# Kernel tuning notes

Measured on AMD Instinct MI355X. Metric: run time of the kernel, lower is better.

## Reference

```python
import jax, jax.numpy as jnp
import numpy as np

N, C, H, W = 16, 256, 48, 96
S = 64   # num_s = 2*num_state_mid; also num_n = mids*mids = 64 (must match)
EPS = 1e-5


def setup_inputs() -> dict:
    key = jax.random.key(0)
    ks = jax.random.split(key, 11)
    sc = 0.05
    return {
        "x": jax.random.normal(ks[0], (N, C, H, W), jnp.float32),
        "edge": jax.random.normal(ks[1], (N, 2, H, W), jnp.float32),
        # conv_state: Conv2d(C, S, 1) with bias
        "Ws": jax.random.normal(ks[2], (S, C), jnp.float32) * sc,
        "bs": jax.random.normal(ks[3], (S,), jnp.float32) * sc,
        # conv_proj: Conv2d(C, S, 1) with bias
        "Wp": jax.random.normal(ks[4], (S, C), jnp.float32) * sc,
        "bp": jax.random.normal(ks[5], (S,), jnp.float32) * sc,
        # GCN conv1: Conv1d(num_n, num_n, 1, bias=False)
        "W1": jax.random.normal(ks[6], (S, S), jnp.float32) * sc,
        # GCN conv2: Conv1d(S, S, 1, bias=False)
        "W2": jax.random.normal(ks[7], (S, S), jnp.float32) * sc,
        # conv_extend: Conv2d(S, C, 1, bias=False)
        "We": jax.random.normal(ks[8], (C, S), jnp.float32) * sc,
        # BatchNorm2d(C) affine params (training-mode batch stats used in forward)
        "gamma": jnp.ones((C,), jnp.float32),
        "beta": jnp.zeros((C,), jnp.float32),
    }


def reference(x, edge, Ws, bs, Wp, bp, W1, W2, We, gamma, beta):
    n, c, h, w = x.shape
    s = Ws.shape[0]
    # edge softmax over channels, take class-1 probability map  -> (n,1,h,w)
    edge_g = jax.nn.softmax(edge, axis=1)[:, 1:2]

    # 1x1 convs as channel matmuls
    xs = jnp.einsum('oc,nchw->nohw', Ws, x) + bs[None, :, None, None]
    xs = xs.reshape(n, s, h * w)                        # (n,S,HW)
    xp = jnp.einsum('oc,nchw->nohw', Wp, x) + bp[None, :, None, None]
    # x_proj_region + x_proj_edge == xp * (1 + edge_gate)
    comb = (xp * (1.0 + edge_g)).reshape(n, s, h * w)
    comb = jax.nn.softmax(comb, axis=-1)                # softmax over spatial

    # project to graph space: (n,S,HW) @ (n,HW,S) -> (n,S,S)
    xn = jnp.einsum('nsk,ntk->nst', xs, comb)

    # GCN: conv1 over node dim (last axis mixes via W1), subtract, conv2 over state dim, relu
    hh = jnp.einsum('ij,nsj->nsi', W1, xn) - xn
    hh = jax.nn.relu(jnp.einsum('ij,njk->nik', W2, hh))

    # back-project: (n,S,S) @ (n,S,HW) -> (n,S,HW) -> (n,S,H,W)
    xr = jnp.einsum('nst,ntk->nsk', hh, comb).reshape(n, s, h, w)

    # conv_extend (no bias) then BatchNorm2d in training mode (biased batch var)
    ext = jnp.einsum('os,nshw->nohw', We, xr)
    mean = ext.mean(axis=(0, 2, 3), keepdims=True)
    var = ext.var(axis=(0, 2, 3), keepdims=True)
    bn = gamma[None, :, None, None] * (ext - mean) * jax.lax.rsqrt(var + EPS) \
         + beta[None, :, None, None]
    return x + bn
```

## Files before the change

kernel.cpp:

```cpp
#include <hip/hip_runtime.h>

#define HW 4608
#define NB 16
#define CC 256
#define SS 64
#define EPS 1e-5f
#define NSPLIT 24

typedef __attribute__((ext_vector_type(8))) short short8;
typedef __attribute__((ext_vector_type(4))) float f32x4;

__device__ __forceinline__ ushort f2bf(float f) {
    uint u = __float_as_uint(f);
    return (ushort)((u + 0x7FFFu + ((u >> 16) & 1u)) >> 16);
}
__device__ __forceinline__ float bf2f(ushort h) {
    return __uint_as_float(((uint)h) << 16);
}

__global__ __launch_bounds__(256) void k_wf(const float* __restrict__ Ws,
                                            const float* __restrict__ Wp,
                                            ushort* __restrict__ Wf) {
    int idx = blockIdx.x * 256 + threadIdx.x;
    int j = idx & 7, r = (idx >> 3) & 127, kq = (idx >> 10) & 3, cs = idx >> 12;
    int c = cs * 32 + kq * 8 + j;
    float v = (r < 64) ? Ws[r * CC + c] : Wp[(r - 64) * CC + c];
    Wf[idx] = f2bf(v);
}

__global__ __launch_bounds__(256) void k_proj(const float* __restrict__ x,
                                              const ushort* __restrict__ Wf,
                                              const float* __restrict__ bs,
                                              const float* __restrict__ bp,
                                              const float* __restrict__ edge,
                                              ushort* __restrict__ xsb,
                                              ushort* __restrict__ Eb,
                                              float* __restrict__ rsum) {
    __shared__ __align__(16) ushort Bl[4 * 64 * 8];
    int n = blockIdx.y, k0 = blockIdx.x * 64;
    int tid = threadIdx.x, lane = tid & 63, w = tid >> 6;
    int q = lane >> 4, li = lane & 15;
    f32x4 acc[2][4] = {};
    const float* xb = x + (size_t)n * CC * HW + k0 + lane;
    float pf[8];
    uint4 afn[2];
#pragma unroll
    for (int j = 0; j < 8; j++) pf[j] = xb[(size_t)(w * 8 + j) * HW];
#pragma unroll
    for (int mt = 0; mt < 2; mt++)
        afn[mt] = *(const uint4*)&Wf[((0 * 4 + q) * 128 + w * 32 + mt * 16 + li) * 8];
#pragma unroll 1
    for (int cs = 0; cs < 8; cs++) {
        union { ushort u[8]; uint4 v; } tmp;
#pragma unroll
        for (int j = 0; j < 8; j++) tmp.u[j] = f2bf(pf[j]);
        short8 af[2];
        af[0] = *(short8*)&afn[0];
        af[1] = *(short8*)&afn[1];
        *(uint4*)&Bl[(w * 64 + lane) * 8] = tmp.v;
        __syncthreads();
        if (cs < 7) {
#pragma unroll
            for (int j = 0; j < 8; j++)
                pf[j] = xb[(size_t)((cs + 1) * 32 + w * 8 + j) * HW];
#pragma unroll
            for (int mt = 0; mt < 2; mt++)
                afn[mt] = *(const uint4*)&Wf[(((cs + 1) * 4 + q) * 128 + w * 32 + mt * 16 + li) * 8];
        }
        short8 bfr[4];
#pragma unroll
        for (int nt = 0; nt < 4; nt++) {
            uint4 t = *(const uint4*)&Bl[(q * 64 + nt * 16 + li) * 8];
            bfr[nt] = *(short8*)&t;
        }
#pragma unroll
        for (int mt = 0; mt < 2; mt++)
#pragma unroll
            for (int nt = 0; nt < 4; nt++)
                acc[mt][nt] = __builtin_amdgcn_mfma_f32_16x16x32_bf16(af[mt], bfr[nt], acc[mt][nt], 0, 0, 0);
        __syncthreads();
    }
    if (w < 2) {
#pragma unroll
        for (int mt = 0; mt < 2; mt++) {
#pragma unroll
            for (int rr = 0; rr < 4; rr++) {
                int s = w * 32 + mt * 16 + q * 4 + rr;
                float bv = bs[s];
#pragma unroll
                for (int nt = 0; nt < 4; nt++) {
                    int col = k0 + nt * 16 + li;
                    xsb[((size_t)n * SS + s) * HW + col] = f2bf(acc[mt][nt][rr] + bv);
                }
            }
        }
    } else {
        float ga[4];
#pragma unroll
        for (int nt = 0; nt < 4; nt++) {
            int col = k0 + nt * 16 + li;
            float e0 = edge[((size_t)n * 2 + 0) * HW + col];
            float e1 = edge[((size_t)n * 2 + 1) * HW + col];
            ga[nt] = 1.f + 1.f / (1.f + __expf(e0 - e1));
        }
        float rp[2][4];
#pragma unroll
        for (int mt = 0; mt < 2; mt++) {
#pragma unroll
            for (int rr = 0; rr < 4; rr++) {
                int s = (w - 2) * 32 + mt * 16 + q * 4 + rr;
                float bv = bp[s];
                float sum = 0.f;
#pragma unroll
                for (int nt = 0; nt < 4; nt++) {
                    int col = k0 + nt * 16 + li;
                    float e = __expf((acc[mt][nt][rr] + bv) * ga[nt]);
                    sum += e;
                    Eb[((size_t)n * SS + s) * HW + col] = f2bf(e);
                }
                rp[mt][rr] = sum;
            }
        }
#pragma unroll
        for (int b = 1; b < 16; b <<= 1)
#pragma unroll
            for (int mt = 0; mt < 2; mt++)
#pragma unroll
                for (int rr = 0; rr < 4; rr++)
                    rp[mt][rr] += __shfl_xor(rp[mt][rr], b, 64);
        if (li == 0) {
#pragma unroll
            for (int mt = 0; mt < 2; mt++)
#pragma unroll
                for (int rr = 0; rr < 4; rr++)
                    atomicAdd(&rsum[n * SS + (w - 2) * 32 + mt * 16 + q * 4 + rr], rp[mt][rr]);
        }
    }
}

__global__ __launch_bounds__(256) void k_graph(const ushort* __restrict__ xsb,
                                               const ushort* __restrict__ Eb,
                                               float* __restrict__ U,
                                               float* __restrict__ P) {
    int n = blockIdx.y, sp = blockIdx.x;
    int kbase = sp * (HW / NSPLIT);
    int tid = threadIdx.x, lane = tid & 63, w = tid >> 6;
    int q = lane >> 4, li = lane & 15;
    bool isP = w >= 2;
    int half = w & 1;
    const ushort* Arow = isP ? Eb : xsb;
    f32x4 acc[2][4] = {};
    for (int ks = 0; ks < (HW / NSPLIT) / 32; ks++) {
        int kb = kbase + ks * 32 + q * 8;
        short8 af[2], bfr[4];
#pragma unroll
        for (int mt = 0; mt < 2; mt++) {
            int s = half * 32 + mt * 16 + li;
            uint4 t = *(const uint4*)&Arow[((size_t)n * SS + s) * HW + kb];
            af[mt] = *(short8*)&t;
        }
#pragma unroll
        for (int nt = 0; nt < 4; nt++) {
            int tt = nt * 16 + li;
            uint4 t = *(const uint4*)&Eb[((size_t)n * SS + tt) * HW + kb];
            bfr[nt] = *(short8*)&t;
        }
#pragma unroll
        for (int mt = 0; mt < 2; mt++)
#pragma unroll
            for (int nt = 0; nt < 4; nt++)
                acc[mt][nt] = __builtin_amdgcn_mfma_f32_16x16x32_bf16(af[mt], bfr[nt], acc[mt][nt], 0, 0, 0);
    }
    float* dst = (isP ? P : U) + (size_t)n * 4096;
#pragma unroll
    for (int mt = 0; mt < 2; mt++)
#pragma unroll
        for (int nt = 0; nt < 4; nt++)
#pragma unroll
            for (int rr = 0; rr < 4; rr++) {
                int row = half * 32 + mt * 16 + q * 4 + rr;
                int col = nt * 16 + li;
                atomicAdd(&dst[row * 64 + col], acc[mt][nt][rr]);
            }
}

__global__ __launch_bounds__(256) void k_gcn(const float* __restrict__ U,
                                             const float* __restrict__ rsum,
                                             const float* __restrict__ W1,
                                             const float* __restrict__ W2,
                                             const float* __restrict__ We,
                                             float* __restrict__ M,
                                             ushort* __restrict__ Mf) {
    __shared__ __align__(16) float A[64 * 68];
    __shared__ __align__(16) float B[64 * 68];
    __shared__ __align__(16) float Cb[64 * 68];
    __shared__ float rs[64];
    int n = blockIdx.x;
    int cc = blockIdx.y;
    int tid = threadIdx.x;
    int t0 = tid >> 4, t1 = tid & 15;
    if (tid < 64) rs[tid] = 1.0f / rsum[n * SS + tid];
    __syncthreads();
#pragma unroll
    for (int i = 0; i < 16; i++) {
        int idx = tid + i * 256;
        int r = idx >> 6, cth = idx & 63;
        A[cth * 68 + r] = U[n * 4096 + idx] * rs[cth];
        B[cth * 68 + r] = W1[idx];
    }
    __syncthreads();
    {
        float acc[4][4] = {};
        for (int j = 0; j < 64; j++) {
            float4 a4 = *(const float4*)&A[j * 68 + t0 * 4];
            float4 b4 = *(const float4*)&B[j * 68 + t1 * 4];
            float a[4] = {a4.x, a4.y, a4.z, a4.w};
            float b[4] = {b4.x, b4.y, b4.z, b4.w};
#pragma unroll
            for (int p = 0; p < 4; p++)
#pragma unroll
                for (int qq = 0; qq < 4; qq++) acc[p][qq] += a[p] * b[qq];
        }
#pragma unroll
        for (int p = 0; p < 4; p++)
#pragma unroll
            for (int qq = 0; qq < 4; qq++) {
                acc[p][qq] -= A[(t1 * 4 + qq) * 68 + (t0 * 4 + p)];
                Cb[(t0 * 4 + p) * 68 + t1 * 4 + qq] = acc[p][qq];
            }
    }
    __syncthreads();
#pragma unroll
    for (int i = 0; i < 16; i++) {
        int idx = tid + i * 256;
        int r = idx >> 6, cth = idx & 63;
        B[cth * 68 + r] = W2[idx];
    }
    __syncthreads();
    {
        float acc[4][4] = {};
        for (int j = 0; j < 64; j++) {
            float4 a4 = *(const float4*)&B[j * 68 + t0 * 4];
            float4 b4 = *(const float4*)&Cb[j * 68 + t1 * 4];
            float a[4] = {a4.x, a4.y, a4.z, a4.w};
            float b[4] = {b4.x, b4.y, b4.z, b4.w};
#pragma unroll
            for (int p = 0; p < 4; p++)
#pragma unroll
                for (int qq = 0; qq < 4; qq++) acc[p][qq] += a[p] * b[qq];
        }
        __syncthreads();
#pragma unroll
        for (int p = 0; p < 4; p++)
#pragma unroll
            for (int qq = 0; qq < 4; qq++)
                A[(t0 * 4 + p) * 68 + t1 * 4 + qq] = fmaxf(acc[p][qq], 0.f);
    }
    __syncthreads();
#pragma unroll
    for (int i = 0; i < 16; i++) {
        int idx = tid + i * 256;
        int c = idx >> 6, j = idx & 63;
        B[j * 68 + c] = We[(cc * 64 + c) * 64 + j];
    }
    __syncthreads();
    {
        float acc[4][4] = {};
        for (int j = 0; j < 64; j++) {
            float4 a4 = *(const float4*)&B[j * 68 + t0 * 4];
            float4 b4 = *(const float4*)&A[j * 68 + t1 * 4];
            float a[4] = {a4.x, a4.y, a4.z, a4.w};
            float b[4] = {b4.x, b4.y, b4.z, b4.w};
#pragma unroll
            for (int p = 0; p < 4; p++)
#pragma unroll
                for (int qq = 0; qq < 4; qq++) acc[p][qq] += a[p] * b[qq];
        }
#pragma unroll
        for (int p = 0; p < 4; p++) {
            int c = cc * 64 + t0 * 4 + p;
            float v[4];
#pragma unroll
            for (int qq = 0; qq < 4; qq++) v[qq] = acc[p][qq] * rs[t1 * 4 + qq];
            float4 st = {v[0], v[1], v[2], v[3]};
            *(float4*)&M[((size_t)n * CC + c) * 64 + t1 * 4] = st;
#pragma unroll
            for (int qq = 0; qq < 4; qq++) {
                int t = t1 * 4 + qq;
                Mf[(size_t)n * 16384 + ((t >> 3) * 256 + c) * 8 + (t & 7)] = f2bf(v[qq]);
            }
        }
    }
}

__global__ __launch_bounds__(256) void k_stats(const float* __restrict__ M,
                                               const float* __restrict__ P,
                                               const float* __restrict__ rsum,
                                               const float* __restrict__ gamma,
                                               const float* __restrict__ beta,
                                               float* __restrict__ sc,
                                               float* __restrict__ bi) {
    __shared__ float ms[NB][64];
    __shared__ float red[256];
    int c = blockIdx.x;
    int tid = threadIdx.x;
    for (int i = tid; i < NB * 64; i += 256) {
        int n = i >> 6, s = i & 63;
        ms[n][s] = M[((size_t)n * CC + c) * 64 + s];
    }
    __syncthreads();
    float qa = 0.f;
    for (int n = 0; n < NB; n++) {
        const float* Pn = P + n * 4096;
#pragma unroll
        for (int p = 0; p < 16; p++) {
            int e = p * 256 + tid;
            qa += ms[n][e >> 6] * ms[n][e & 63] * Pn[e];
        }
    }
    float sa = 0.f;
    for (int i = tid; i < NB * 64; i += 256) {
        int n = i >> 6, s = i & 63;
        sa += ms[n][s] * rsum[n * SS + s];
    }
    red[tid] = qa;
    __syncthreads();
    for (int off = 128; off > 0; off >>= 1) {
        if (tid < off) red[tid] += red[tid + off];
        __syncthreads();
    }
    float qtot = red[0];
    __syncthreads();
    red[tid] = sa;
    __syncthreads();
    for (int off = 128; off > 0; off >>= 1) {
        if (tid < off) red[tid] += red[tid + off];
        __syncthreads();
    }
    if (tid == 0) {
        float stot = red[0];
        const float invM = 1.0f / ((float)NB * (float)HW);
        float mean = stot * invM;
        float var = qtot * invM - mean * mean;
        float s = gamma[c] * rsqrtf(var + EPS);
        sc[c] = s;
        bi[c] = beta[c] - s * mean;
    }
}

__global__ __launch_bounds__(256) void k_out(const float* __restrict__ x,
                                             const ushort* __restrict__ Mf,
                                             const ushort* __restrict__ Eb,
                                             const float* __restrict__ sc,
                                             const float* __restrict__ bi,
                                             float* __restrict__ out) {
    __shared__ __align__(16) ushort Bl[8 * 64 * 8];
    int n = blockIdx.y, k0 = blockIdx.x * 64;
    int tid = threadIdx.x, lane = tid & 63, w = tid >> 6;
    int q = lane >> 4, li = lane & 15;
    {
        int nl = tid & 63, pr = tid >> 6;
#pragma unroll
        for (int kk = 0; kk < 2; kk++) {
            int kq = pr * 2 + kk;
            union { ushort u[8]; uint4 v; } tmp;
#pragma unroll
            for (int j = 0; j < 8; j++)
                tmp.u[j] = Eb[((size_t)n * SS + kq * 8 + j) * HW + k0 + nl];
            *(uint4*)&Bl[(kq * 64 + nl) * 8] = tmp.v;
        }
    }
    __syncthreads();
    f32x4 acc[4][4] = {};
#pragma unroll
    for (int ks = 0; ks < 2; ks++) {
        short8 af[4], bfr[4];
#pragma unroll
        for (int mt = 0; mt < 4; mt++) {
            int c = w * 64 + mt * 16 + li;
            uint4 t = *(const uint4*)&Mf[(size_t)n * 16384 + ((ks * 4 + q) * 256 + c) * 8];
            af[mt] = *(short8*)&t;
        }
#pragma unroll
        for (int nt = 0; nt < 4; nt++) {
            int nl = nt * 16 + li;
            uint4 t = *(const uint4*)&Bl[((ks * 4 + q) * 64 + nl) * 8];
            bfr[nt] = *(short8*)&t;
        }
#pragma unroll
        for (int mt = 0; mt < 4; mt++)
#pragma unroll
            for (int nt = 0; nt < 4; nt++)
                acc[mt][nt] = __builtin_amdgcn_mfma_f32_16x16x32_bf16(af[mt], bfr[nt], acc[mt][nt], 0, 0, 0);
    }
#pragma unroll
    for (int mt = 0; mt < 4; mt++) {
#pragma unroll
        for (int rr = 0; rr < 4; rr++) {
            int c = w * 64 + mt * 16 + q * 4 + rr;
            float s_ = sc[c], bv = bi[c];
            size_t base = ((size_t)n * CC + c) * HW + k0;
#pragma unroll
            for (int nt = 0; nt < 4; nt++) {
                int col = nt * 16 + li;
                out[base + col] = x[base + col] + s_ * acc[mt][nt][rr] + bv;
            }
        }
    }
}

extern "C" void kernel_launch(void* const* d_in, const int* in_sizes, int n_in,
                              void* d_out, int out_size, void* d_ws, size_t ws_size,
                              hipStream_t stream) {
    const float* x = (const float*)d_in[0];
    const float* edge = (const float*)d_in[1];
    const float* Ws = (const float*)d_in[2];
    const float* bs = (const float*)d_in[3];
    const float* Wp = (const float*)d_in[4];
    const float* bp = (const float*)d_in[5];
    const float* W1 = (const float*)d_in[6];
    const float* W2 = (const float*)d_in[7];
    const float* We = (const float*)d_in[8];
    const float* gamma = (const float*)d_in[9];
    const float* beta = (const float*)d_in[10];
    float* out = (float*)d_out;

    char* base = (char*)d_ws;
    ushort* Wf  = (ushort*)base;                    base += 65536;
    ushort* xsb = (ushort*)base;                    base += 9437184;
    ushort* Eb  = (ushort*)base;                    base += 9437184;
    float*  rsum= (float*)base;                     base += 4096;
    float*  U   = (float*)base;                     base += 262144;
    float*  P   = (float*)base;                     base += 262144;
    float*  M   = (float*)base;                     base += 1048576;
    ushort* Mf  = (ushort*)base;                    base += 524288;
    float*  sc  = (float*)base;                     base += 1024;
    float*  bi  = (float*)base;                     base += 1024;

    hipMemsetAsync(rsum, 0, 4096 + 262144 + 262144, stream);
    k_wf<<<128, 256, 0, stream>>>(Ws, Wp, Wf);
    k_proj<<<dim3(72, NB), 256, 0, stream>>>(x, Wf, bs, bp, edge, xsb, Eb, rsum);
    k_graph<<<dim3(NSPLIT, NB), 256, 0, stream>>>(xsb, Eb, U, P);
    k_gcn<<<dim3(NB, 4), 256, 0, stream>>>(U, rsum, W1, W2, We, M, Mf);
    k_stats<<<256, 256, 0, stream>>>(M, P, rsum, gamma, beta, sc, bi);
    k_out<<<dim3(72, NB), 256, 0, stream>>>(x, Mf, Eb, sc, bi, out);
}
```

Measured before the change: 223.4 us.

## Double-buffer projection LDS tile and vectorize output epilogue through shared staging

```diff
diff --git a/kernel.cpp b/kernel.cpp
--- a/kernel.cpp
+++ b/kernel.cpp
@@ -36,7 +36,7 @@
                                               ushort* __restrict__ xsb,
                                               ushort* __restrict__ Eb,
                                               float* __restrict__ rsum) {
-    __shared__ __align__(16) ushort Bl[4 * 64 * 8];
+    __shared__ __align__(16) ushort Bl[2][4 * 64 * 8];
     int n = blockIdx.y, k0 = blockIdx.x * 64;
     int tid = threadIdx.x, lane = tid & 63, w = tid >> 6;
     int q = lane >> 4, li = lane & 15;
@@ -49,16 +49,18 @@
 #pragma unroll
     for (int mt = 0; mt < 2; mt++)
         afn[mt] = *(const uint4*)&Wf[((0 * 4 + q) * 128 + w * 32 + mt * 16 + li) * 8];
-#pragma unroll 1
+#pragma unroll 2
     for (int cs = 0; cs < 8; cs++) {
+        int b = cs & 1;
         union { ushort u[8]; uint4 v; } tmp;
 #pragma unroll
         for (int j = 0; j < 8; j++) tmp.u[j] = f2bf(pf[j]);
         short8 af[2];
         af[0] = *(short8*)&afn[0];
         af[1] = *(short8*)&afn[1];
-        *(uint4*)&Bl[(w * 64 + lane) * 8] = tmp.v;
-        __syncthreads();
+        *(uint4*)&Bl[b][(w * 64 + lane) * 8] = tmp.v;
+        asm volatile("s_waitcnt lgkmcnt(0)" ::: "memory");
+        __builtin_amdgcn_s_barrier();
         if (cs < 7) {
 #pragma unroll
             for (int j = 0; j < 8; j++)
@@ -70,7 +72,7 @@
         short8 bfr[4];
 #pragma unroll
         for (int nt = 0; nt < 4; nt++) {
-            uint4 t = *(const uint4*)&Bl[(q * 64 + nt * 16 + li) * 8];
+            uint4 t = *(const uint4*)&Bl[b][(q * 64 + nt * 16 + li) * 8];
             bfr[nt] = *(short8*)&t;
         }
 #pragma unroll
@@ -78,7 +80,6 @@
 #pragma unroll
             for (int nt = 0; nt < 4; nt++)
                 acc[mt][nt] = __builtin_amdgcn_mfma_f32_16x16x32_bf16(af[mt], bfr[nt], acc[mt][nt], 0, 0, 0);
-        __syncthreads();
     }
     if (w < 2) {
 #pragma unroll
@@ -354,57 +355,73 @@
                                              const float* __restrict__ sc,
                                              const float* __restrict__ bi,
                                              float* __restrict__ out) {
-    __shared__ __align__(16) ushort Bl[8 * 64 * 8];
-    int n = blockIdx.y, k0 = blockIdx.x * 64;
+    __shared__ __align__(16) char shb[64 * 132 * 4];
+    ushort* Bl = (ushort*)shb;
+    float* E2 = (float*)shb;
+    int n = blockIdx.y;
+    int kt = blockIdx.x >> 1, ct = blockIdx.x & 1;
+    int k0 = kt * 128, c0 = ct * 128;
     int tid = threadIdx.x, lane = tid & 63, w = tid >> 6;
     int q = lane >> 4, li = lane & 15;
     {
-        int nl = tid & 63, pr = tid >> 6;
-#pragma unroll
-        for (int kk = 0; kk < 2; kk++) {
-            int kq = pr * 2 + kk;
+        int nl = tid & 127, pr = tid >> 7;
+#pragma unroll
+        for (int kk = 0; kk < 4; kk++) {
+            int kq = pr * 4 + kk;
             union { ushort u[8]; uint4 v; } tmp;
 #pragma unroll
             for (int j = 0; j < 8; j++)
                 tmp.u[j] = Eb[((size_t)n * SS + kq * 8 + j) * HW + k0 + nl];
-            *(uint4*)&Bl[(kq * 64 + nl) * 8] = tmp.v;
-        }
-    }
-    __syncthreads();
-    f32x4 acc[4][4] = {};
+            *(uint4*)&Bl[(kq * 128 + nl) * 8] = tmp.v;
+        }
+    }
+    __syncthreads();
+    f32x4 acc[2][8] = {};
 #pragma unroll
     for (int ks = 0; ks < 2; ks++) {
-        short8 af[4], bfr[4];
-#pragma unroll
-        for (int mt = 0; mt < 4; mt++) {
-            int c = w * 64 + mt * 16 + li;
+        short8 af[2], bfr[8];
+#pragma unroll
+        for (int mt = 0; mt < 2; mt++) {
+            int c = c0 + w * 32 + mt * 16 + li;
             uint4 t = *(const uint4*)&Mf[(size_t)n * 16384 + ((ks * 4 + q) * 256 + c) * 8];
             af[mt] = *(short8*)&t;
         }
 #pragma unroll
-        for (int nt = 0; nt < 4; nt++) {
+        for (int nt = 0; nt < 8; nt++) {
             int nl = nt * 16 + li;
-            uint4 t = *(const uint4*)&Bl[((ks * 4 + q) * 64 + nl) * 8];
+            uint4 t = *(const uint4*)&Bl[((ks * 4 + q) * 128 + nl) * 8];
             bfr[nt] = *(short8*)&t;
         }
 #pragma unroll
-        for (int mt = 0; mt < 4; mt++)
-#pragma unroll
-            for (int nt = 0; nt < 4; nt++)
+        for (int mt = 0; mt < 2; mt++)
+#pragma unroll
+            for (int nt = 0; nt < 8; nt++)
                 acc[mt][nt] = __builtin_amdgcn_mfma_f32_16x16x32_bf16(af[mt], bfr[nt], acc[mt][nt], 0, 0, 0);
     }
-#pragma unroll
-    for (int mt = 0; mt < 4; mt++) {
-#pragma unroll
-        for (int rr = 0; rr < 4; rr++) {
-            int c = w * 64 + mt * 16 + q * 4 + rr;
+#pragma unroll 1
+    for (int mtc = 0; mtc < 2; mtc++) {
+        __syncthreads();
+#pragma unroll
+        for (int nt = 0; nt < 8; nt++)
+#pragma unroll
+            for (int rr = 0; rr < 4; rr++)
+                E2[(w * 16 + q * 4 + rr) * 132 + nt * 16 + li] = acc[mtc][nt][rr];
+        __syncthreads();
+#pragma unroll
+        for (int i = 0; i < 8; i++) {
+            int r = (tid >> 5) + i * 8;
+            int c4 = tid & 31;
+            int c = c0 + (r >> 4) * 32 + mtc * 16 + (r & 15);
             float s_ = sc[c], bv = bi[c];
-            size_t base = ((size_t)n * CC + c) * HW + k0;
-#pragma unroll
-            for (int nt = 0; nt < 4; nt++) {
-                int col = nt * 16 + li;
-                out[base + col] = x[base + col] + s_ * acc[mt][nt][rr] + bv;
-            }
+            float4 av = *(const float4*)&E2[r * 132 + c4 * 4];
+            size_t base = ((size_t)n * CC + c) * HW + k0 + c4 * 4;
+            float4 xv = *(const float4*)&x[base];
+            float4 o;
+            o.x = xv.x + s_ * av.x + bv;
+            o.y = xv.y + s_ * av.y + bv;
+            o.z = xv.z + s_ * av.z + bv;
+            o.w = xv.w + s_ * av.w + bv;
+            *(float4*)&out[base] = o;
         }
     }
 }
```

After: 266.9 us. +19.4%, slower.
